# Performance work log

Hardware: AMD Instinct MI355X
Metric: run time of the kernel (lower is better)

## Reference

```python
import jax, jax.numpy as jnp
import numpy as np

B, S, D, H = 8, 128, 256, 8
T = S + 1
HD = D // H  # head_dim = 32
GAMMA = 1.0
NEG_INF = -1e9
LN_EPS = 1e-5


def setup_inputs() -> dict:
    key = jax.random.key(0)
    ks = jax.random.split(key, 16)
    sc = 0.05
    return {
        "desc_embeddings": jax.random.normal(ks[0], (B, S, D), jnp.float32),
        "name_value_embeddings": jax.random.normal(ks[1], (B, T, D), jnp.float32),
        "prior_Q": jax.random.uniform(ks[2], (B, H, S, S), jnp.float32),
        "Wq": jax.random.normal(ks[3], (D, D), jnp.float32) * sc,
        "bq": jnp.zeros((D,), jnp.float32),
        "Wk": jax.random.normal(ks[4], (D, D), jnp.float32) * sc,
        "bk": jnp.zeros((D,), jnp.float32),
        "Wv": jax.random.normal(ks[5], (D, D), jnp.float32) * sc,
        "bv": jnp.zeros((D,), jnp.float32),
        "wa": jax.random.normal(ks[6], (3 * HD,), jnp.float32) * sc,  # attn_proj weight (out=1)
        "ba": jnp.zeros((), jnp.float32),
        "We1": jax.random.normal(ks[7], (2 * D, D), jnp.float32) * sc,
        "be1": jnp.zeros((D,), jnp.float32),
        "ln_g": jnp.ones((D,), jnp.float32),
        "ln_b": jnp.zeros((D,), jnp.float32),
        "We2": jax.random.normal(ks[8], (D, D), jnp.float32) * sc,
        "be2": jnp.zeros((D,), jnp.float32),
    }


def _layer_norm(x, g, b):
    mu = jnp.mean(x, axis=-1, keepdims=True)
    var = jnp.mean(jnp.square(x - mu), axis=-1, keepdims=True)
    return (x - mu) * jax.lax.rsqrt(var + LN_EPS) * g + b


def _heads(x, W, b):  # [B,T,D] -> [B,H,T,HD]
    return (x @ W + b).reshape(B, T, H, HD).transpose(0, 2, 1, 3)


def reference(desc_embeddings, name_value_embeddings, prior_Q,
              Wq, bq, Wk, bk, Wv, bv, wa, ba,
              We1, be1, ln_g, ln_b, We2, be2):
    # structural adjacency (same for every batch element): CLS->Var on, Var->CLS off,
    # Var-Var fully connected without self-loops
    adj = jnp.zeros((T, T), jnp.float32)
    adj = adj.at[1:, 1:].set(1.0 - jnp.eye(S, dtype=jnp.float32))
    adj = adj.at[0, 1:].set(1.0)

    q = _heads(name_value_embeddings, Wq, bq)  # [B,H,T,HD]
    k = _heads(name_value_embeddings, Wk, bk)
    v = _heads(name_value_embeddings, Wv, bv)

    # edge attributes: pairwise concat of desc embeddings, CLS rows/cols use [desc,desc]
    desc = desc_embeddings
    var_edge = jnp.concatenate([
        jnp.broadcast_to(desc[:, :, None, :], (B, S, S, D)),
        jnp.broadcast_to(desc[:, None, :, :], (B, S, S, D)),
    ], axis=-1)  # [B,S,S,2D]
    cls_edge = jnp.concatenate([desc, desc], axis=-1)  # [B,S,2D]
    edge = jnp.zeros((B, T, T, 2 * D), jnp.float32)
    edge = edge.at[:, 1:, 1:].set(var_edge)
    edge = edge.at[:, 0, 1:].set(cls_edge)
    edge = edge.at[:, 1:, 0].set(cls_edge)

    # edge_update MLP: Linear(2D->D) -> LayerNorm -> ReLU -> Linear(D->D)
    h = jax.nn.relu(_layer_norm(edge @ We1 + be1, ln_g, ln_b)) @ We2 + be2  # [B,T,T,D]
    # split into heads, mask by adjacency: [B,H,T,T,HD]
    edge_h = h.reshape(B, T, T, H, HD).transpose(0, 3, 1, 2, 4)
    edge_h = edge_h * adj[None, None, :, :, None]

    # gat_v1 + attn_proj(cat[q_i, k_j, e_ij]) is linear -> decompose to avoid
    # materializing the [B,H,T,T,3*HD] concat
    wa_q, wa_k, wa_e = wa[:HD], wa[HD:2 * HD], wa[2 * HD:]
    logits = (jnp.einsum('bhid,d->bhi', q, wa_q)[:, :, :, None]
              + jnp.einsum('bhjd,d->bhj', k, wa_k)[:, :, None, :]
              + jnp.einsum('bhijd,d->bhij', edge_h, wa_e)
              + ba)  # [B,H,T,T]

    # prior_Q logit-bias injection on Var-Var block
    eps = 1e-6
    p = jnp.clip(prior_Q, eps, 1.0 - eps)
    bias = (jnp.log(p) - jnp.log(1.0 - p)) * GAMMA  # [B,H,S,S]
    logits = logits.at[:, :, 1:, 1:].add(bias)

    # structural mask as pre-softmax -inf
    logits = logits + (adj == 0).astype(logits.dtype)[None, None] * NEG_INF

    attn = jax.nn.softmax(logits, axis=-1)  # [B,H,T,T]
    ctx = jnp.einsum('bhij,bhjd->bhid', attn, v)  # [B,H,T,HD]
    basis_outputs = ctx.transpose(0, 2, 1, 3)  # [B,T,H,HD]
    return basis_outputs, attn
```

## Files before the change

kernel.cpp:

```cpp
#include <hip/hip_runtime.h>
#include <math.h>

#define B 8
#define S 128
#define D 256
#define H 8
#define T 129
#define HD 32
#define NEG_INF -1000000000.0f
#define LN_EPS 1e-5f

__global__ __launch_bounds__(256) void prep_w(
    const float* __restrict__ Wq, const float* __restrict__ bq,
    const float* __restrict__ Wk, const float* __restrict__ bk,
    const float* __restrict__ We2, const float* __restrict__ be2,
    const float* __restrict__ wa,
    float* __restrict__ Wqk, float* __restrict__ bqk,
    float* __restrict__ W2aT, float* __restrict__ econst)
{
    int id = blockIdx.x * 256 + threadIdx.x;
    if (id < 2048) {
        int c = id >> 3, h = id & 7;
        float s = 0.f;
        #pragma unroll
        for (int d = 0; d < HD; ++d) s = fmaf(Wq[c*D + h*HD + d], wa[d], s);
        Wqk[c*16 + h] = s;
    } else if (id < 4096) {
        int id2 = id - 2048; int c = id2 >> 3, h = id2 & 7;
        float s = 0.f;
        #pragma unroll
        for (int d = 0; d < HD; ++d) s = fmaf(Wk[c*D + h*HD + d], wa[HD + d], s);
        Wqk[c*16 + 8 + h] = s;
    } else if (id < 6144) {
        int id2 = id - 4096; int h = id2 / D, c = id2 % D;
        float s = 0.f;
        #pragma unroll
        for (int d = 0; d < HD; ++d) s = fmaf(We2[c*D + h*HD + d], wa[2*HD + d], s);
        W2aT[h*D + c] = s;
    } else if (id < 6152) {
        int h = id - 6144;
        float s = 0.f;
        #pragma unroll
        for (int d = 0; d < HD; ++d) s = fmaf(bq[h*HD + d], wa[d], s);
        bqk[h] = s;
    } else if (id < 6160) {
        int h = id - 6152;
        float s = 0.f;
        #pragma unroll
        for (int d = 0; d < HD; ++d) s = fmaf(bk[h*HD + d], wa[HD + d], s);
        bqk[8 + h] = s;
    } else if (id < 6168) {
        int h = id - 6160;
        float s = 0.f;
        #pragma unroll
        for (int d = 0; d < HD; ++d) s = fmaf(be2[h*HD + d], wa[2*HD + d], s);
        econst[h] = s;
    }
}

__global__ __launch_bounds__(256) void gemm3(
    const float* __restrict__ nv, const float* __restrict__ desc,
    const float* __restrict__ Wv, const float* __restrict__ bv,
    const float* __restrict__ We1, const float* __restrict__ be1,
    float* __restrict__ v, float* __restrict__ U, float* __restrict__ V)
{
    const int which = blockIdx.y;
    const float* X; const float* W; const float* bias; float* out; int rows;
    if (which == 0)      { X = nv;   W = Wv;        bias = bv;  out = v; rows = B*T; }
    else if (which == 1) { X = desc; W = We1;       bias = be1; out = U; rows = B*S; }
    else                 { X = desc; W = We1 + D*D; bias = nullptr; out = V; rows = B*S; }

    const int r0  = blockIdx.x * 8;
    const int tid = threadIdx.x;
    __shared__ float xs[8][D];

    #pragma unroll
    for (int r = 0; r < 8; ++r) {
        int rr = r0 + r;
        xs[r][tid] = (rr < rows) ? X[rr * D + tid] : 0.f;
    }
    __syncthreads();

    float acc[8] = {0.f,0.f,0.f,0.f,0.f,0.f,0.f,0.f};
    for (int kk = 0; kk < D; kk += 4) {
        float w0 = W[(kk+0)*D + tid];
        float w1 = W[(kk+1)*D + tid];
        float w2 = W[(kk+2)*D + tid];
        float w3 = W[(kk+3)*D + tid];
        #pragma unroll
        for (int r = 0; r < 8; ++r) {
            float4 x = *(const float4*)&xs[r][kk];
            acc[r] = fmaf(x.x, w0, acc[r]);
            acc[r] = fmaf(x.y, w1, acc[r]);
            acc[r] = fmaf(x.z, w2, acc[r]);
            acc[r] = fmaf(x.w, w3, acc[r]);
        }
    }
    const float bb = bias ? bias[tid] : 0.f;
    #pragma unroll
    for (int r = 0; r < 8; ++r) {
        int rr = r0 + r;
        if (rr < rows) out[rr * D + tid] = acc[r] + bb;
    }
}

__global__ __launch_bounds__(256) void qdkd_gemm(
    const float* __restrict__ nv, const float* __restrict__ Wqk,
    const float* __restrict__ bqk, float* __restrict__ qdkd)
{
    const int r0 = blockIdx.x * 16;
    const int tid = threadIdx.x;
    const int r = tid >> 4, c = tid & 15;
    __shared__ float xs[16][D];

    for (int t = tid; t < 16 * D; t += 256) {
        int rr = r0 + (t >> 8);
        xs[t >> 8][t & 255] = (rr < B*T) ? nv[rr * D + (t & 255)] : 0.f;
    }
    __syncthreads();

    float acc = 0.f;
    for (int kk = 0; kk < D; kk += 4) {
        float4 x = *(const float4*)&xs[r][kk];
        acc = fmaf(x.x, Wqk[(kk+0)*16 + c], acc);
        acc = fmaf(x.y, Wqk[(kk+1)*16 + c], acc);
        acc = fmaf(x.z, Wqk[(kk+2)*16 + c], acc);
        acc = fmaf(x.w, Wqk[(kk+3)*16 + c], acc);
    }
    const int rr = r0 + r;
    if (rr < B*T) qdkd[rr * 16 + c] = acc + bqk[c];
}

__global__ __launch_bounds__(512) void edge_attn(
    const float* __restrict__ U, const float* __restrict__ V,
    const float* __restrict__ W2aT, const float* __restrict__ econst,
    const float* __restrict__ ln_g, const float* __restrict__ ln_b,
    const float* __restrict__ qdkd, const float* __restrict__ prior,
    const float* __restrict__ v, const float* __restrict__ ba,
    float* __restrict__ out_basis, float* __restrict__ out_attn)
{
    const int bid = blockIdx.x;
    const int b = bid / T, i = bid % T;
    const int tid = threadIdx.x, lane = tid & 63, wid = tid >> 6;
    const int c0 = lane * 4;

    __shared__ float escl[H][132];
    __shared__ float pat[H][132];

    const float4 g4 = *(const float4*)(ln_g + c0);
    const float4 b4 = *(const float4*)(ln_b + c0);
    float4 w[H];
    #pragma unroll
    for (int h = 0; h < H; ++h) w[h] = *(const float4*)(W2aT + h*D + c0);
    float4 u4i = make_float4(0.f, 0.f, 0.f, 0.f);
    if (i >= 1) u4i = *(const float4*)(U + (b*S + (i-1))*D + c0);

    const int hmap = 4*(lane&1) + 2*((lane>>1)&1) + ((lane>>2)&1);
    const float ecl = (lane < 8) ? econst[hmap] : 0.f;

    const int j0 = 1 + wid * 16;
    for (int jj = 0; jj < 16; ++jj) {
        const int j = j0 + jj;
        if (i >= 1 && j == i) continue;

        const float4 v4 = *(const float4*)(V + (b*S + (j-1))*D + c0);
        float4 u4;
        if (i == 0) u4 = *(const float4*)(U + (b*S + (j-1))*D + c0);
        else        u4 = u4i;

        const float y0 = u4.x + v4.x, y1 = u4.y + v4.y;
        const float y2 = u4.z + v4.z, y3 = u4.w + v4.w;

        float s1 = y0 + y1 + y2 + y3;
        float s2 = fmaf(y0, y0, fmaf(y1, y1, fmaf(y2, y2, y3 * y3)));
        #pragma unroll
        for (int m = 32; m >= 1; m >>= 1) {
            s1 += __shfl_xor(s1, m);
            s2 += __shfl_xor(s2, m);
        }
        const float mu  = s1 * (1.f / D);
        const float var = s2 * (1.f / D) - mu * mu;
        const float rs  = rsqrtf(var + LN_EPS);

        const float t0 = fmaxf((y0 - mu) * rs * g4.x + b4.x, 0.f);
        const float t1 = fmaxf((y1 - mu) * rs * g4.y + b4.y, 0.f);
        const float t2 = fmaxf((y2 - mu) * rs * g4.z + b4.z, 0.f);
        const float t3 = fmaxf((y3 - mu) * rs * g4.w + b4.w, 0.f);

        float ph[H];
        #pragma unroll
        for (int h = 0; h < H; ++h)
            ph[h] = fmaf(t0, w[h].x, fmaf(t1, w[h].y, fmaf(t2, w[h].z, t3 * w[h].w)));

        {
            const bool hi = (lane & 1);
            float k0 = hi ? ph[4] : ph[0], d0 = hi ? ph[0] : ph[4];
            float k1 = hi ? ph[5] : ph[1], d1 = hi ? ph[1] : ph[5];
            float k2 = hi ? ph[6] : ph[2], d2 = hi ? ph[2] : ph[6];
            float k3 = hi ? ph[7] : ph[3], d3 = hi ? ph[3] : ph[7];
            ph[0] = k0 + __shfl_xor(d0, 1);
            ph[1] = k1 + __shfl_xor(d1, 1);
            ph[2] = k2 + __shfl_xor(d2, 1);
            ph[3] = k3 + __shfl_xor(d3, 1);
        }
        {
            const bool hi = (lane & 2);
            float k0 = hi ? ph[2] : ph[0], d0 = hi ? ph[0] : ph[2];
            float k1 = hi ? ph[3] : ph[1], d1 = hi ? ph[1] : ph[3];
            ph[0] = k0 + __shfl_xor(d0, 2);
            ph[1] = k1 + __shfl_xor(d1, 2);
        }
        {
            const bool hi = (lane & 4);
            float k0 = hi ? ph[1] : ph[0], d0 = hi ? ph[0] : ph[1];
            ph[0] = k0 + __shfl_xor(d0, 4);
        }
        ph[0] += __shfl_xor(ph[0], 8);
        ph[0] += __shfl_xor(ph[0], 16);
        ph[0] += __shfl_xor(ph[0], 32);

        if (lane < 8) escl[hmap][j] = ph[0] + ecl;
    }
    __syncthreads();

    const int h = wid;
    const int bh = b*H + h;
    const float qdv = qdkd[(b*T + i)*16 + h];
    const float ba0 = ba[0];
    const int j1 = 1 + lane, j2 = 65 + lane;
    const bool v1 = !(i >= 1 && j1 == i);
    const bool v2 = !(i >= 1 && j2 == i);

    float l1 = NEG_INF, l2 = NEG_INF;
    if (v1) {
        l1 = qdv + qdkd[(b*T + j1)*16 + 8 + h] + escl[h][j1] + ba0;
        if (i >= 1) {
            float pr = prior[(bh*S + (i-1))*S + (j1-1)];
            pr = fminf(fmaxf(pr, 1e-6f), 1.f - 1e-6f);
            l1 += logf(pr) - logf(1.f - pr);
        }
    }
    if (v2) {
        l2 = qdv + qdkd[(b*T + j2)*16 + 8 + h] + escl[h][j2] + ba0;
        if (i >= 1) {
            float pr = prior[(bh*S + (i-1))*S + (j2-1)];
            pr = fminf(fmaxf(pr, 1e-6f), 1.f - 1e-6f);
            l2 += logf(pr) - logf(1.f - pr);
        }
    }

    float m = fmaxf(l1, l2);
    #pragma unroll
    for (int mm = 32; mm >= 1; mm >>= 1) m = fmaxf(m, __shfl_xor(m, mm));
    const float e1 = v1 ? expf(l1 - m) : 0.f;
    const float e2 = v2 ? expf(l2 - m) : 0.f;
    float s = e1 + e2;
    #pragma unroll
    for (int mm = 32; mm >= 1; mm >>= 1) s += __shfl_xor(s, mm);
    const float inv = 1.f / s;
    const float a1 = e1 * inv, a2 = e2 * inv;

    float* arow = out_attn + (size_t)(bh*T + i)*T;
    arow[j1] = a1;
    arow[j2] = a2;
    if (lane == 0) arow[0] = 0.f;
    pat[h][j1] = a1;
    pat[h][j2] = a2;
    __syncthreads();

    const int d = lane & 31, half = lane >> 5;
    float acc = 0.f;
    const float* vb = v + (size_t)(b*T)*D + h*HD + d;
    #pragma unroll 4
    for (int jj = 0; jj < 64; ++jj) {
        const int j = 1 + half*64 + jj;
        acc = fmaf(pat[h][j], vb[j*D], acc);
    }
    acc += __shfl_xor(acc, 32);
    if (lane < 32)
        out_basis[((b*T + i)*H + h)*HD + d] = acc;
}

extern "C" void kernel_launch(void* const* d_in, const int* in_sizes, int n_in,
                              void* d_out, int out_size, void* d_ws, size_t ws_size,
                              hipStream_t stream) {
    const float* desc  = (const float*)d_in[0];
    const float* nv    = (const float*)d_in[1];
    const float* prior = (const float*)d_in[2];
    const float* Wq  = (const float*)d_in[3];
    const float* bq  = (const float*)d_in[4];
    const float* Wk  = (const float*)d_in[5];
    const float* bk  = (const float*)d_in[6];
    const float* Wv  = (const float*)d_in[7];
    const float* bv  = (const float*)d_in[8];
    const float* wa  = (const float*)d_in[9];
    const float* ba  = (const float*)d_in[10];
    const float* We1 = (const float*)d_in[11];
    const float* be1 = (const float*)d_in[12];
    const float* lng = (const float*)d_in[13];
    const float* lnb = (const float*)d_in[14];
    const float* We2 = (const float*)d_in[15];
    const float* be2 = (const float*)d_in[16];

    float* ws = (float*)d_ws;
    float* U    = ws; ws += B*S*D;
    float* V    = ws; ws += B*S*D;
    float* v    = ws; ws += B*T*D;
    float* Wqk  = ws; ws += D*16;
    float* bqk  = ws; ws += 16;
    float* W2aT = ws; ws += H*D;
    float* ec   = ws; ws += H;
    float* qdkd = ws; ws += B*T*16;

    float* out_basis = (float*)d_out;
    float* out_attn  = out_basis + B*T*H*HD;

    prep_w<<<dim3(25), 256, 0, stream>>>(Wq, bq, Wk, bk, We2, be2, wa,
                                         Wqk, bqk, W2aT, ec);
    gemm3<<<dim3(129, 3), 256, 0, stream>>>(nv, desc, Wv, bv, We1, be1, v, U, V);
    qdkd_gemm<<<dim3(65), 256, 0, stream>>>(nv, Wqk, bqk, qdkd);
    edge_attn<<<dim3(B*T), 512, 0, stream>>>(U, V, W2aT, ec, lng, lnb,
                                             qdkd, prior, v, ba,
                                             out_basis, out_attn);
}
```

Before: 174.3 us.

## Merge weight prep and projection GEMMs into one kernel launch

```diff
diff --git a/kernel.cpp b/kernel.cpp
--- a/kernel.cpp
+++ b/kernel.cpp
@@ -10,125 +10,141 @@
 #define NEG_INF -1000000000.0f
 #define LN_EPS 1e-5f
 
-__global__ __launch_bounds__(256) void prep_w(
+__global__ __launch_bounds__(256) void gemm_all(
+    const float* __restrict__ nv, const float* __restrict__ desc,
     const float* __restrict__ Wq, const float* __restrict__ bq,
     const float* __restrict__ Wk, const float* __restrict__ bk,
+    const float* __restrict__ Wv, const float* __restrict__ bv,
+    const float* __restrict__ We1, const float* __restrict__ be1,
     const float* __restrict__ We2, const float* __restrict__ be2,
     const float* __restrict__ wa,
-    float* __restrict__ Wqk, float* __restrict__ bqk,
-    float* __restrict__ W2aT, float* __restrict__ econst)
+    float* __restrict__ v, float* __restrict__ U, float* __restrict__ V,
+    float* __restrict__ qdkd, float* __restrict__ W2aT, float* __restrict__ econst)
 {
-    int id = blockIdx.x * 256 + threadIdx.x;
-    if (id < 2048) {
-        int c = id >> 3, h = id & 7;
-        float s = 0.f;
-        #pragma unroll
-        for (int d = 0; d < HD; ++d) s = fmaf(Wq[c*D + h*HD + d], wa[d], s);
-        Wqk[c*16 + h] = s;
-    } else if (id < 4096) {
-        int id2 = id - 2048; int c = id2 >> 3, h = id2 & 7;
-        float s = 0.f;
-        #pragma unroll
-        for (int d = 0; d < HD; ++d) s = fmaf(Wk[c*D + h*HD + d], wa[HD + d], s);
-        Wqk[c*16 + 8 + h] = s;
-    } else if (id < 6144) {
-        int id2 = id - 4096; int h = id2 / D, c = id2 % D;
-        float s = 0.f;
-        #pragma unroll
-        for (int d = 0; d < HD; ++d) s = fmaf(We2[c*D + h*HD + d], wa[2*HD + d], s);
-        W2aT[h*D + c] = s;
-    } else if (id < 6152) {
-        int h = id - 6144;
-        float s = 0.f;
-        #pragma unroll
-        for (int d = 0; d < HD; ++d) s = fmaf(bq[h*HD + d], wa[d], s);
-        bqk[h] = s;
-    } else if (id < 6160) {
-        int h = id - 6152;
-        float s = 0.f;
-        #pragma unroll
-        for (int d = 0; d < HD; ++d) s = fmaf(bk[h*HD + d], wa[HD + d], s);
-        bqk[8 + h] = s;
-    } else if (id < 6168) {
-        int h = id - 6160;
-        float s = 0.f;
-        #pragma unroll
-        for (int d = 0; d < HD; ++d) s = fmaf(be2[h*HD + d], wa[2*HD + d], s);
-        econst[h] = s;
-    }
-}
-
-__global__ __launch_bounds__(256) void gemm3(
-    const float* __restrict__ nv, const float* __restrict__ desc,
-    const float* __restrict__ Wv, const float* __restrict__ bv,
-    const float* __restrict__ We1, const float* __restrict__ be1,
-    float* __restrict__ v, float* __restrict__ U, float* __restrict__ V)
-{
-    const int which = blockIdx.y;
-    const float* X; const float* W; const float* bias; float* out; int rows;
-    if (which == 0)      { X = nv;   W = Wv;        bias = bv;  out = v; rows = B*T; }
-    else if (which == 1) { X = desc; W = We1;       bias = be1; out = U; rows = B*S; }
-    else                 { X = desc; W = We1 + D*D; bias = nullptr; out = V; rows = B*S; }
-
-    const int r0  = blockIdx.x * 8;
+    const int blk = blockIdx.x;
     const int tid = threadIdx.x;
-    __shared__ float xs[8][D];
-
-    #pragma unroll
-    for (int r = 0; r < 8; ++r) {
-        int rr = r0 + r;
-        xs[r][tid] = (rr < rows) ? X[rr * D + tid] : 0.f;
-    }
-    __syncthreads();
-
-    float acc[8] = {0.f,0.f,0.f,0.f,0.f,0.f,0.f,0.f};
-    for (int kk = 0; kk < D; kk += 4) {
-        float w0 = W[(kk+0)*D + tid];
-        float w1 = W[(kk+1)*D + tid];
-        float w2 = W[(kk+2)*D + tid];
-        float w3 = W[(kk+3)*D + tid];
+
+    __shared__ float xs[16][260];
+    __shared__ float wq_s[256 * 16];
+    __shared__ float bq_s[16];
+
+    if (blk < 193) {
+        const float* X; const float* W; const float* bias; float* out; int rows; int r0;
+        if (blk < 65)       { X = nv;   W = Wv;        bias = bv;      out = v; rows = B*T; r0 = blk * 16; }
+        else if (blk < 129) { X = desc; W = We1;       bias = be1;     out = U; rows = B*S; r0 = (blk - 65) * 16; }
+        else                { X = desc; W = We1 + D*D; bias = nullptr; out = V; rows = B*S; r0 = (blk - 129) * 16; }
+
+        for (int t = tid; t < 16 * 256; t += 256) {
+            const int r = t >> 8, c = t & 255, rr = r0 + r;
+            xs[r][c] = (rr < rows) ? X[rr * D + c] : 0.f;
+        }
+        __syncthreads();
+
+        const int c  = tid & 127;
+        const int rg = (tid >> 7) * 8;
+
+        float acc[8][2];
+        #pragma unroll
+        for (int r = 0; r < 8; ++r) { acc[r][0] = 0.f; acc[r][1] = 0.f; }
+
+        float wA[8], wB[8], nA[8], nB[8];
+        #pragma unroll
+        for (int q = 0; q < 8; ++q) { wA[q] = W[q*D + c]; wB[q] = W[q*D + c + 128]; }
+
+        for (int kk = 0; kk < 256; kk += 8) {
+            const int kn = kk + 8;
+            if (kn < 256) {
+                #pragma unroll
+                for (int q = 0; q < 8; ++q) {
+                    nA[q] = W[(kn + q)*D + c];
+                    nB[q] = W[(kn + q)*D + c + 128];
+                }
+            }
+            #pragma unroll
+            for (int qh = 0; qh < 8; qh += 4) {
+                #pragma unroll
+                for (int r = 0; r < 8; ++r) {
+                    const float4 x = *(const float4*)&xs[rg + r][kk + qh];
+                    acc[r][0] = fmaf(x.x, wA[qh+0], acc[r][0]);
+                    acc[r][0] = fmaf(x.y, wA[qh+1], acc[r][0]);
+                    acc[r][0] = fmaf(x.z, wA[qh+2], acc[r][0]);
+                    acc[r][0] = fmaf(x.w, wA[qh+3], acc[r][0]);
+                    acc[r][1] = fmaf(x.x, wB[qh+0], acc[r][1]);
+                    acc[r][1] = fmaf(x.y, wB[qh+1], acc[r][1]);
+                    acc[r][1] = fmaf(x.z, wB[qh+2], acc[r][1]);
+                    acc[r][1] = fmaf(x.w, wB[qh+3], acc[r][1]);
+                }
+            }
+            if (kn < 256) {
+                #pragma unroll
+                for (int q = 0; q < 8; ++q) { wA[q] = nA[q]; wB[q] = nB[q]; }
+            }
+        }
+
+        const float b0 = bias ? bias[c]       : 0.f;
+        const float b1 = bias ? bias[c + 128] : 0.f;
         #pragma unroll
         for (int r = 0; r < 8; ++r) {
-            float4 x = *(const float4*)&xs[r][kk];
-            acc[r] = fmaf(x.x, w0, acc[r]);
-            acc[r] = fmaf(x.y, w1, acc[r]);
-            acc[r] = fmaf(x.z, w2, acc[r]);
-            acc[r] = fmaf(x.w, w3, acc[r]);
-        }
-    }
-    const float bb = bias ? bias[tid] : 0.f;
-    #pragma unroll
-    for (int r = 0; r < 8; ++r) {
-        int rr = r0 + r;
-        if (rr < rows) out[rr * D + tid] = acc[r] + bb;
-    }
-}
-
-__global__ __launch_bounds__(256) void qdkd_gemm(
-    const float* __restrict__ nv, const float* __restrict__ Wqk,
-    const float* __restrict__ bqk, float* __restrict__ qdkd)
-{
-    const int r0 = blockIdx.x * 16;
-    const int tid = threadIdx.x;
-    const int r = tid >> 4, c = tid & 15;
-    __shared__ float xs[16][D];
-
-    for (int t = tid; t < 16 * D; t += 256) {
-        int rr = r0 + (t >> 8);
-        xs[t >> 8][t & 255] = (rr < B*T) ? nv[rr * D + (t & 255)] : 0.f;
-    }
-    __syncthreads();
-
-    float acc = 0.f;
-    for (int kk = 0; kk < D; kk += 4) {
-        float4 x = *(const float4*)&xs[r][kk];
-        acc = fmaf(x.x, Wqk[(kk+0)*16 + c], acc);
-        acc = fmaf(x.y, Wqk[(kk+1)*16 + c], acc);
-        acc = fmaf(x.z, Wqk[(kk+2)*16 + c], acc);
-        acc = fmaf(x.w, Wqk[(kk+3)*16 + c], acc);
-    }
-    const int rr = r0 + r;
-    if (rr < B*T) qdkd[rr * 16 + c] = acc + bqk[c];
+            const int rr = r0 + rg + r;
+            if (rr < rows) {
+                out[rr * D + c]       = acc[r][0] + b0;
+                out[rr * D + c + 128] = acc[r][1] + b1;
+            }
+        }
+    } else if (blk < 258) {
+        const int r0 = (blk - 193) * 16;
+
+        for (int t = tid; t < 4096; t += 256) {
+            const int k = t >> 4, cc = t & 15;
+            const float* Wsrc = (cc < 8) ? Wq : Wk;
+            const float* wap  = (cc < 8) ? wa : wa + HD;
+            const int h = cc & 7;
+            float s = 0.f;
+            #pragma unroll
+            for (int d = 0; d < HD; ++d) s = fmaf(Wsrc[k*D + h*HD + d], wap[d], s);
+            wq_s[t] = s;
+        }
+        if (tid < 16) {
+            const float* bsrc = (tid < 8) ? bq : bk;
+            const float* wap  = (tid < 8) ? wa : wa + HD;
+            const int h = tid & 7;
+            float s = 0.f;
+            #pragma unroll
+            for (int d = 0; d < HD; ++d) s = fmaf(bsrc[h*HD + d], wap[d], s);
+            bq_s[tid] = s;
+        }
+        for (int t = tid; t < 16 * 256; t += 256) {
+            const int r = t >> 8, c = t & 255, rr = r0 + r;
+            xs[r][c] = (rr < B*T) ? nv[rr * D + c] : 0.f;
+        }
+        __syncthreads();
+
+        const int r = tid >> 4, cc = tid & 15;
+        float acc = 0.f;
+        for (int kk = 0; kk < 256; kk += 4) {
+            const float4 x = *(const float4*)&xs[r][kk];
+            acc = fmaf(x.x, wq_s[(kk+0)*16 + cc], acc);
+            acc = fmaf(x.y, wq_s[(kk+1)*16 + cc], acc);
+            acc = fmaf(x.z, wq_s[(kk+2)*16 + cc], acc);
+            acc = fmaf(x.w, wq_s[(kk+3)*16 + cc], acc);
+        }
+        const int rr = r0 + r;
+        if (rr < B*T) qdkd[rr * 16 + cc] = acc + bq_s[cc];
+    } else {
+        for (int t = tid; t < 2048; t += 256) {
+            const int h = t >> 8, c = t & 255;
+            float s = 0.f;
+            #pragma unroll
+            for (int d = 0; d < HD; ++d) s = fmaf(We2[c*D + h*HD + d], wa[2*HD + d], s);
+            W2aT[h*D + c] = s;
+        }
+        if (tid < 8) {
+            float s = 0.f;
+            #pragma unroll
+            for (int d = 0; d < HD; ++d) s = fmaf(be2[tid*HD + d], wa[2*HD + d], s);
+            econst[tid] = s;
+        }
+    }
 }
 
 __global__ __launch_bounds__(512) void edge_attn(
@@ -306,8 +322,6 @@
     float* U    = ws; ws += B*S*D;
     float* V    = ws; ws += B*S*D;
     float* v    = ws; ws += B*T*D;
-    float* Wqk  = ws; ws += D*16;
-    float* bqk  = ws; ws += 16;
     float* W2aT = ws; ws += H*D;
     float* ec   = ws; ws += H;
     float* qdkd = ws; ws += B*T*16;
@@ -315,10 +329,9 @@
     float* out_basis = (float*)d_out;
     float* out_attn  = out_basis + B*T*H*HD;
 
-    prep_w<<<dim3(25), 256, 0, stream>>>(Wq, bq, Wk, bk, We2, be2, wa,
-                                         Wqk, bqk, W2aT, ec);
-    gemm3<<<dim3(129, 3), 256, 0, stream>>>(nv, desc, Wv, bv, We1, be1, v, U, V);
-    qdkd_gemm<<<dim3(65), 256, 0, stream>>>(nv, Wqk, bqk, qdkd);
+    gemm_all<<<dim3(259), 256, 0, stream>>>(nv, desc, Wq, bq, Wk, bk, Wv, bv,
+                                            We1, be1, We2, be2, wa,
+                                            v, U, V, qdkd, W2aT, ec);
     edge_attn<<<dim3(B*T), 512, 0, stream>>>(U, V, W2aT, ec, lng, lnb,
                                              qdkd, prior, v, ba,
                                              out_basis, out_attn);
```

Measured after the change: 178.0 us. +2.1%, slower.
